# Kernel optimization log

Measured on AMD Instinct MI355X. Metric: run time of the kernel, lower is better.

## Reference

```python
import jax, jax.numpy as jnp
import numpy as np

B = 4096
NQ = 4  # qubits -> 16-dim state vector


def _make_ops(seed, n_ops):
    # Deterministic stand-in for tq.RandomLayer: random RX/RY/RZ/CRX gates.
    rng = np.random.default_rng(seed)
    ops = []
    for _ in range(n_ops):
        kind = int(rng.integers(0, 4))
        if kind == 3:  # CRX on two distinct wires
            w = rng.choice(NQ, size=2, replace=False)
            ops.append((3, int(w[0]), int(w[1])))
        else:
            ops.append((kind, int(rng.integers(0, NQ)), 0))
    return ops

ENC_OPS = _make_ops(1, 8)    # QuantumPatchEncoder.random_layer (n_ops=8)
QFC_OPS = _make_ops(2, 50)   # QuantumFullyConnectedLayer.random_layer (n_ops=50)

_H = np.array([[1, 1], [1, -1]], np.complex64) * np.complex64(1.0 / np.sqrt(2.0))
_SX = np.array([[1 + 1j, 1 - 1j], [1 - 1j, 1 + 1j]], np.complex64) * np.complex64(0.5)
_CNOT = np.array([[1, 0, 0, 0], [0, 1, 0, 0], [0, 0, 0, 1], [0, 0, 1, 0]], np.complex64)


def _rx(t):
    c = jnp.cos(t / 2) + 0j
    s = -1j * jnp.sin(t / 2)
    return jnp.stack([jnp.stack([c, s], -1), jnp.stack([s, c], -1)], -2)


def _ry(t):
    c = jnp.cos(t / 2) + 0j
    s = jnp.sin(t / 2) + 0j
    return jnp.stack([jnp.stack([c, -s], -1), jnp.stack([s, c], -1)], -2)


def _rz(t):
    e0 = jnp.exp(-1j * t / 2)
    e1 = jnp.exp(1j * t / 2)
    z = jnp.zeros_like(e0)
    return jnp.stack([jnp.stack([e0, z], -1), jnp.stack([z, e1], -1)], -2)


def _crx(t):
    return jnp.eye(4, dtype=jnp.complex64).at[2:, 2:].set(_rx(t))


def _apply1(state, U, w):
    # state: (B, 2,2,2,2); U: (2,2) or per-sample (B,2,2)
    state = jnp.moveaxis(state, w + 1, -1)
    if U.ndim == 3:
        state = jnp.einsum('b...i,bji->b...j', state, U)
    else:
        state = jnp.einsum('...i,ji->...j', state, U)
    return jnp.moveaxis(state, -1, w + 1)


def _apply2(state, U, w0, w1):
    state = jnp.moveaxis(state, (w0 + 1, w1 + 1), (-2, -1))
    shp = state.shape
    state = state.reshape(shp[:-2] + (4,)) @ U.T
    return jnp.moveaxis(state.reshape(shp), (-2, -1), (w0 + 1, w1 + 1))


def _random_layer(state, ops, params):
    for i, (kind, w0, w1) in enumerate(ops):
        t = params[i]
        if kind == 0:
            state = _apply1(state, _rx(t), w0)
        elif kind == 1:
            state = _apply1(state, _ry(t), w0)
        elif kind == 2:
            state = _apply1(state, _rz(t), w0)
        else:
            state = _apply2(state, _crx(t), w0, w1)
    return state


def _measure_z(state):
    # <Z> on each wire from |amp|^2 marginals
    probs = state.real ** 2 + state.imag ** 2
    exps = []
    for w in range(NQ):
        axes = tuple(a for a in range(1, NQ + 1) if a != w + 1)
        m = probs.sum(axes)  # (B, 2)
        exps.append(m[:, 0] - m[:, 1])
    return jnp.stack(exps, 1)


def _conv(x, W, b):
    y = jax.lax.conv_general_dilated(x, W, (1, 1), 'SAME',
                                     dimension_numbers=('NCHW', 'OIHW', 'NCHW'))
    return y + b[None, :, None, None]


def _pool(x):
    return jax.lax.reduce_window(x, -jnp.inf, jax.lax.max,
                                 (1, 1, 2, 2), (1, 1, 2, 2), 'VALID')


def setup_inputs() -> dict:
    key = jax.random.key(0)
    ks = jax.random.split(key, 8)
    f = lambda k, shp, fan: jax.random.normal(k, shp, jnp.float32) / np.float32(np.sqrt(fan))
    two_pi = float(2 * np.pi)
    return {
        'x': jax.random.uniform(ks[0], (B, 1, 32, 32), jnp.float32),
        'conv1_w': f(ks[1], (8, 1, 3, 3), 9),
        'conv1_b': jnp.zeros((8,), jnp.float32),
        'conv2_w': f(ks[2], (16, 8, 3, 3), 72),
        'conv2_b': jnp.zeros((16,), jnp.float32),
        'enc_params': jax.random.uniform(ks[3], (8,), jnp.float32, 0.0, two_pi),
        'qfc_rand_params': jax.random.uniform(ks[4], (50,), jnp.float32, 0.0, two_pi),
        'qfc_params': jax.random.uniform(ks[5], (4,), jnp.float32, 0.0, two_pi),
        'bn_gamma': jnp.ones((4,), jnp.float32),
        'bn_beta': jnp.zeros((4,), jnp.float32),
        'fc_w': f(ks[6], (10, 68), 68),
        'fc_b': jnp.zeros((10,), jnp.float32),
    }


def reference(x, conv1_w, conv1_b, conv2_w, conv2_b, enc_params, qfc_rand_params,
              qfc_params, bn_gamma, bn_beta, fc_w, fc_b):
    # CNN feature extractor
    h = _pool(jax.nn.relu(_conv(x, conv1_w, conv1_b)))
    h = _pool(jax.nn.relu(_conv(h, conv2_w, conv2_b)))  # (B, 16, 8, 8)
    b = h.shape[0]
    pm = h.mean(1)  # channel-mean, (B, 8, 8)
    # 2x2 patches, row-major within patch, scanning r then c -> (B, 16, 4)
    patches = pm.reshape(b, 4, 2, 4, 2).transpose(0, 1, 3, 2, 4).reshape(b, 16, 4)

    # Encoder: fresh |0000> per patch (GeneralEncoder resets state); batch all
    # B*16 patch circuits together instead of looping.
    data = patches.reshape(b * 16, 4)
    state = jnp.zeros((b * 16, 16), jnp.complex64).at[:, 0].set(1.0)
    state = state.reshape(b * 16, 2, 2, 2, 2)
    for w in range(NQ):
        state = _apply1(state, _ry(data[:, w]), w)
    state = _random_layer(state, ENC_OPS, enc_params)
    qfeat = _measure_z(state).reshape(b, 64)  # (B, 16*4)

    # QFC operates on the state left by the LAST patch (as in the original)
    s = state.reshape(b, 16, 2, 2, 2, 2)[:, 15]
    s = _random_layer(s, QFC_OPS, qfc_rand_params)
    s = _apply1(s, _rx(qfc_params[0]), 0)
    s = _apply1(s, _ry(qfc_params[1]), 1)
    s = _apply1(s, _rz(qfc_params[2]), 3)
    s = _apply2(s, _crx(qfc_params[3]), 0, 2)
    s = _apply1(s, jnp.asarray(_H), 3)
    s = _apply1(s, jnp.asarray(_SX), 2)
    s = _apply2(s, jnp.asarray(_CNOT), 3, 0)
    q = _measure_z(s)  # (B, 4)

    # BatchNorm1d(4), training-mode (batch stats, biased var)
    mu = q.mean(0)
    var = q.var(0)
    q = (q - mu) / jnp.sqrt(var + 1e-5) * bn_gamma + bn_beta

    feats = jnp.concatenate([qfeat, q], 1)  # (B, 68)
    logits = feats @ fc_w.T + fc_b
    return jax.nn.log_softmax(logits, -1)
```

## Files before the change

kernel.cpp:

```cpp
#include <hip/hip_runtime.h>
#include <cstdint>

namespace crng {

typedef unsigned __int128 u128;

struct PCG {
    u128 state, inc;
    bool has32;
    uint32_t buf32;
};

constexpr u128 PCG_MULT = (((u128)2549297995355413924ULL) << 64) | (u128)4865540595714422341ULL;

constexpr uint64_t pcg_next64(PCG& g) {
    g.state = g.state * PCG_MULT + g.inc;
    uint64_t hi = (uint64_t)(g.state >> 64), lo = (uint64_t)g.state;
    unsigned rot = (unsigned)(g.state >> 122) & 63u;
    uint64_t v = hi ^ lo;
    return (v >> rot) | (v << ((64u - rot) & 63u));
}

constexpr uint32_t pcg_next32(PCG& g) {
    if (g.has32) { g.has32 = false; return g.buf32; }
    uint64_t n = pcg_next64(g);
    g.has32 = true;
    g.buf32 = (uint32_t)(n >> 32);
    return (uint32_t)n;
}

constexpr uint32_t hashmix(uint32_t& hc, uint32_t v) {
    v ^= hc; hc *= 0x931e8875u; v *= hc; v ^= v >> 16; return v;
}
constexpr uint32_t mixf(uint32_t x, uint32_t y) {
    uint32_t r = 0xca01f9ddu * x - 0x4973f715u * y;
    r ^= r >> 16;
    return r;
}

constexpr PCG seed_pcg(uint32_t entropy) {
    uint32_t pool[4] = {0, 0, 0, 0};
    uint32_t hc = 0x43b0d7e5u;
    pool[0] = hashmix(hc, entropy);
    for (int i = 1; i < 4; ++i) pool[i] = hashmix(hc, 0u);
    for (int s = 0; s < 4; ++s)
        for (int d = 0; d < 4; ++d)
            if (s != d) pool[d] = mixf(pool[d], hashmix(hc, pool[s]));

    uint32_t hb = 0x8b51f9ddu;
    uint32_t w[8] = {0, 0, 0, 0, 0, 0, 0, 0};
    for (int i = 0; i < 8; ++i) {
        uint32_t dv = pool[i & 3];
        dv ^= hb; hb *= 0x58f38dedu; dv *= hb; dv ^= dv >> 16;
        w[i] = dv;
    }
    uint64_t w64[4] = {0, 0, 0, 0};
    for (int i = 0; i < 4; ++i)
        w64[i] = (uint64_t)w[2 * i] | ((uint64_t)w[2 * i + 1] << 32);

    u128 initstate = (((u128)w64[0]) << 64) | (u128)w64[1];
    u128 initseq   = (((u128)w64[2]) << 64) | (u128)w64[3];
    PCG g = {};
    g.state = 0;
    g.inc = (initseq << 1) | (u128)1;
    g.state = g.state * PCG_MULT + g.inc;
    g.state += initstate;
    g.state = g.state * PCG_MULT + g.inc;
    g.has32 = false;
    g.buf32 = 0;
    return g;
}

constexpr uint32_t lemire32(PCG& g, uint32_t rng) {
    uint64_t rng_excl = (uint64_t)rng + 1;
    uint64_t m = (uint64_t)pcg_next32(g) * rng_excl;
    uint32_t leftover = (uint32_t)m;
    if (leftover < (uint32_t)rng_excl) {
        uint32_t threshold = (uint32_t)((uint64_t)(0xFFFFFFFFu - rng) % rng_excl);
        while (leftover < threshold) {
            m = (uint64_t)pcg_next32(g) * rng_excl;
            leftover = (uint32_t)m;
        }
    }
    return (uint32_t)(m >> 32);
}

struct Ops {
    int enc[8];
    int qfc[50];
};

constexpr void fill_ops(PCG& g, int n, int* out) {
    for (int i = 0; i < n; ++i) {
        uint32_t kind = lemire32(g, 3);
        uint32_t w0 = 0, w1 = 0;
        if (kind == 3) {
            uint32_t v2 = lemire32(g, 2);
            uint32_t v3 = lemire32(g, 3);
            uint32_t a0 = v2;
            uint32_t a1 = (v3 == v2) ? 3u : v3;
            uint32_t j = lemire32(g, 1);
            if (j == 0) { uint32_t t = a0; a0 = a1; a1 = t; }
            w0 = a0; w1 = a1;
        } else {
            w0 = lemire32(g, 3);
        }
        out[i] = (int)((kind << 4) | (w0 << 2) | w1);
    }
}

constexpr Ops make_ops_ct() {
    Ops o = {};
    PCG g1 = seed_pcg(1u);
    fill_ops(g1, 8, o.enc);
    PCG g2 = seed_pcg(2u);
    fill_ops(g2, 50, o.qfc);
    return o;
}

}

constexpr crng::Ops kOps = crng::make_ops_ct();

typedef _Float16 half8 __attribute__((ext_vector_type(8)));
typedef float float4v __attribute__((ext_vector_type(4)));

#define XS_STRIDE 24
#define XS_PLANE  (34 * XS_STRIDE)
#define XS_TOT    (2 * XS_PLANE)
#define H1F_ROW   (18 * 8)

__global__ __launch_bounds__(256, 4) void cnn_kernel(
    const float* __restrict__ x, const float* __restrict__ w1,
    const float* __restrict__ b1, const float* __restrict__ w2,
    const float* __restrict__ b2, float* __restrict__ pm,
    float* __restrict__ stats)
{
    __shared__ float xs[XS_TOT];
    __shared__ __align__(16) _Float16 h1f[18 * H1F_ROW];
    __shared__ __align__(16) _Float16 Ahalf[9 * 16 * 8];
    __shared__ float w1s[72], b1s[8], b2s[16];

    const int tid = threadIdx.x;
    const int b = blockIdx.x;
    const float* xb = x + (size_t)b * 1024;

    for (int k = tid; k < XS_TOT; k += 256) xs[k] = 0.f;
    for (int k = tid; k < 18 * H1F_ROW; k += 256) h1f[k] = (_Float16)0.f;
    for (int e = tid; e < 1152; e += 256) {
        int uv = e >> 7, m = (e >> 3) & 15, ci = e & 7;
        Ahalf[e] = (_Float16)w2[m * 72 + ci * 9 + uv];
    }
    if (tid < 72) w1s[tid] = w1[tid];
    if (tid < 8) b1s[tid] = b1[tid];
    if (tid < 16) b2s[tid] = b2[tid];
    if (b == 0 && tid < 8) stats[tid] = 0.f;
    __syncthreads();

    for (int k = tid; k < 1024; k += 256) {
        int r = k >> 5, c = k & 31;
        int p = c & 1;
        int q = p ? ((c + 1) >> 1) : (c >> 1);
        xs[p * XS_PLANE + (r + 1) * XS_STRIDE + q] = xb[k];
    }
    __syncthreads();

    {
        const int i = tid >> 4, j = tid & 15;
        float patch[4][4];
#pragma unroll
        for (int u = 0; u < 4; ++u) {
            int r = 2 * i + u;
            const float* ev = &xs[r * XS_STRIDE + j];
            const float* od = &xs[XS_PLANE + r * XS_STRIDE + j];
            patch[u][0] = od[0];
            patch[u][1] = ev[0];
            patch[u][2] = od[1];
            patch[u][3] = ev[1];
        }
        half8 hv;
#pragma unroll
        for (int c = 0; c < 8; ++c) {
            float m = -3.4e38f;
#pragma unroll
            for (int di = 0; di < 2; ++di)
#pragma unroll
                for (int dj = 0; dj < 2; ++dj) {
                    float acc = b1s[c];
#pragma unroll
                    for (int u = 0; u < 3; ++u)
#pragma unroll
                        for (int v = 0; v < 3; ++v)
                            acc += w1s[c * 9 + u * 3 + v] * patch[di + u][dj + v];
                    m = fmaxf(m, acc);
                }
            hv[c] = (_Float16)fmaxf(m, 0.f);
        }
        *(half8*)&h1f[(i + 1) * H1F_ROW + (j + 1) * 8] = hv;
    }
    __syncthreads();

    {
        const int w = tid >> 6;
        const int lane = tid & 63;
        const int pj = lane & 15;
        const int quad = lane >> 4;

        half8 afrag[9];
#pragma unroll
        for (int uv = 0; uv < 9; ++uv) {
            half8 a = {};
            if (quad == 0) a = *(const half8*)&Ahalf[(uv * 16 + pj) * 8];
            afrag[uv] = a;
        }

        float4v acc[4];
#pragma unroll
        for (int tl = 0; tl < 4; ++tl) {
            float4v c;
#pragma unroll
            for (int r = 0; r < 4; ++r) c[r] = b2s[4 * quad + r];
            acc[tl] = c;
        }

#pragma unroll
        for (int tl = 0; tl < 4; ++tl) {
            const int t = 4 * w + tl;
#pragma unroll
            for (int u = 0; u < 3; ++u) {
#pragma unroll
                for (int v = 0; v < 3; ++v) {
                    half8 bf = *(const half8*)&h1f[(t + u) * H1F_ROW + (pj + v) * 8];
                    acc[tl] = __builtin_amdgcn_mfma_f32_16x16x32_f16(
                        afrag[u * 3 + v], bf, acc[tl], 0, 0, 0);
                }
            }
        }

#pragma unroll
        for (int p = 0; p < 2; ++p) {
            float4v m1;
#pragma unroll
            for (int r = 0; r < 4; ++r)
                m1[r] = fmaxf(acc[2 * p][r], acc[2 * p + 1][r]);
            float s = 0.f;
#pragma unroll
            for (int r = 0; r < 4; ++r) {
                float o = __shfl_xor((float)m1[r], 1, 64);
                float mv = fmaxf(fmaxf(m1[r], o), 0.f);
                s += mv;
            }
            s += __shfl_xor(s, 16, 64);
            s += __shfl_xor(s, 32, 64);
            if (quad == 0 && !(pj & 1)) {
                const int i2 = 2 * w + p, j2 = pj >> 1;
                pm[(size_t)b * 64 + i2 * 8 + j2] = s * (1.f / 16.f);
            }
        }
    }
}

template<int KIND, int W0, int W1>
__device__ __forceinline__ void gate_ct(float (&ur)[16], float (&ui)[16],
                                        float ch, float sh)
{
    constexpr bool CTRL = (KIND == 3 || KIND == 6);
    constexpr int STT = CTRL ? (8 >> W1) : (8 >> W0);
    constexpr int STC = CTRL ? (8 >> W0) : 0;
#pragma unroll
    for (int k0 = 0; k0 < 16; ++k0) {
        if (k0 & STT) continue;
        if (STC != 0 && !(k0 & STC)) continue;
        const int k1 = k0 | STT;
        float x0r = ur[k0], x0i = ui[k0], x1r = ur[k1], x1i = ui[k1];
        if constexpr (KIND == 0 || KIND == 3) {
            ur[k0] = ch * x0r + sh * x1i;  ui[k0] = ch * x0i - sh * x1r;
            ur[k1] = sh * x0i + ch * x1r;  ui[k1] = -sh * x0r + ch * x1i;
        } else if constexpr (KIND == 1) {
            ur[k0] = ch * x0r - sh * x1r;  ui[k0] = ch * x0i - sh * x1i;
            ur[k1] = sh * x0r + ch * x1r;  ui[k1] = sh * x0i + ch * x1i;
        } else if constexpr (KIND == 2) {
            ur[k0] = ch * x0r + sh * x0i;  ui[k0] = ch * x0i - sh * x0r;
            ur[k1] = ch * x1r - sh * x1i;  ui[k1] = ch * x1i + sh * x1r;
        } else if constexpr (KIND == 4) {
            constexpr float RH = 0.70710678118654752f;
            ur[k0] = RH * (x0r + x1r);  ui[k0] = RH * (x0i + x1i);
            ur[k1] = RH * (x0r - x1r);  ui[k1] = RH * (x0i - x1i);
        } else if constexpr (KIND == 5) {
            ur[k0] = 0.5f * (x0r + x1r) - 0.5f * x0i + 0.5f * x1i;
            ui[k0] = 0.5f * (x0i + x1i) + 0.5f * x0r - 0.5f * x1r;
            ur[k1] = 0.5f * (x0r + x1r) + 0.5f * x0i - 0.5f * x1i;
            ui[k1] = 0.5f * (x0i + x1i) - 0.5f * x0r + 0.5f * x1r;
        } else {
            ur[k0] = x1r; ui[k0] = x1i;
            ur[k1] = x0r; ui[k1] = x0i;
        }
    }
}

template<int I>
__device__ __forceinline__ void run_enc(float (&ur)[16], float (&ui)[16],
                                        const float* ch, const float* sh)
{
    if constexpr (I < 8) {
        constexpr int op = kOps.enc[I];
        gate_ct<(op >> 4) & 7, (op >> 2) & 3, op & 3>(ur, ui, ch[I], sh[I]);
        run_enc<I + 1>(ur, ui, ch, sh);
    }
}

template<int I>
__device__ __forceinline__ void run_qfc(float (&ur)[16], float (&ui)[16],
                                        const float* ch, const float* sh)
{
    if constexpr (I < 50) {
        constexpr int op = kOps.qfc[I];
        gate_ct<(op >> 4) & 7, (op >> 2) & 3, op & 3>(ur, ui, ch[I], sh[I]);
        run_qfc<I + 1>(ur, ui, ch, sh);
    }
}

__global__ __launch_bounds__(256) void quantum_kernel(
    const float* __restrict__ pm, const float* __restrict__ encp,
    const float* __restrict__ qfcr, const float* __restrict__ qfcp,
    float* __restrict__ qfeat, float* __restrict__ qraw,
    float* __restrict__ stats, int Bv)
{
    __shared__ float chs[62], shs[62];
    __shared__ float rstat[128];

    const int tid = threadIdx.x;
    if (tid < 62) {
        float t = (tid < 8) ? encp[tid] : (tid < 58) ? qfcr[tid - 8] : qfcp[tid - 58];
        chs[tid] = cosf(0.5f * t);
        shs[tid] = sinf(0.5f * t);
    }
    __syncthreads();

    const int gid = blockIdx.x * 256 + tid;
    const int b = gid >> 4, p = gid & 15;
    float qq[4] = {0.f, 0.f, 0.f, 0.f};
    bool last = false;

    if (b < Bv) {
        const int pr = p >> 2, pc = p & 3;
        const float* pmb = pm + (size_t)b * 64;
        float d0 = pmb[(2 * pr) * 8 + 2 * pc];
        float d1 = pmb[(2 * pr) * 8 + 2 * pc + 1];
        float d2 = pmb[(2 * pr + 1) * 8 + 2 * pc];
        float d3 = pmb[(2 * pr + 1) * 8 + 2 * pc + 1];
        float f0c = cosf(0.5f * d0), f0s = sinf(0.5f * d0);
        float f1c = cosf(0.5f * d1), f1s = sinf(0.5f * d1);
        float f2c = cosf(0.5f * d2), f2s = sinf(0.5f * d2);
        float f3c = cosf(0.5f * d3), f3s = sinf(0.5f * d3);

        float ur[16], ui[16];
#pragma unroll
        for (int k = 0; k < 16; ++k) {
            float v = ((k & 8) ? f0s : f0c);
            v *= ((k & 4) ? f1s : f1c);
            v *= ((k & 2) ? f2s : f2c);
            v *= ((k & 1) ? f3s : f3c);
            ur[k] = v;
            ui[k] = 0.f;
        }
        run_enc<0>(ur, ui, chs, shs);

        float qv[4] = {0.f, 0.f, 0.f, 0.f};
#pragma unroll
        for (int k = 0; k < 16; ++k) {
            float pk = ur[k] * ur[k] + ui[k] * ui[k];
            qv[0] += (k & 8) ? -pk : pk;
            qv[1] += (k & 4) ? -pk : pk;
            qv[2] += (k & 2) ? -pk : pk;
            qv[3] += (k & 1) ? -pk : pk;
        }
        *(float4*)(qfeat + (size_t)b * 64 + p * 4) = make_float4(qv[0], qv[1], qv[2], qv[3]);

        if (p == 15) {
            last = true;
            run_qfc<0>(ur, ui, chs + 8, shs + 8);
            gate_ct<0, 0, 0>(ur, ui, chs[58], shs[58]);
            gate_ct<1, 1, 0>(ur, ui, chs[59], shs[59]);
            gate_ct<2, 3, 0>(ur, ui, chs[60], shs[60]);
            gate_ct<3, 0, 2>(ur, ui, chs[61], shs[61]);
            gate_ct<4, 3, 0>(ur, ui, 0.f, 0.f);
            gate_ct<5, 2, 0>(ur, ui, 0.f, 0.f);
            gate_ct<6, 3, 0>(ur, ui, 0.f, 0.f);
#pragma unroll
            for (int k = 0; k < 16; ++k) {
                float pk = ur[k] * ur[k] + ui[k] * ui[k];
                qq[0] += (k & 8) ? -pk : pk;
                qq[1] += (k & 4) ? -pk : pk;
                qq[2] += (k & 2) ? -pk : pk;
                qq[3] += (k & 1) ? -pk : pk;
            }
            *(float4*)(qraw + (size_t)b * 4) = make_float4(qq[0], qq[1], qq[2], qq[3]);
        }
    }

    for (int k = tid; k < 128; k += 256) rstat[k] = 0.f;
    __syncthreads();
    const int m = tid >> 4;
    if (last) {
#pragma unroll
        for (int w = 0; w < 4; ++w) {
            rstat[w * 16 + m] = qq[w];
            rstat[64 + w * 16 + m] = qq[w] * qq[w];
        }
    }
    __syncthreads();
    if (tid < 8) {
        float s = 0.f;
#pragma unroll
        for (int k = 0; k < 16; ++k) s += rstat[tid * 16 + k];
        atomicAdd(&stats[tid], s);
    }
}

__global__ __launch_bounds__(256) void head_kernel(
    const float* __restrict__ qfeat, const float* __restrict__ qraw,
    const float* __restrict__ stats, const float* __restrict__ gam,
    const float* __restrict__ bet, const float* __restrict__ fcw,
    const float* __restrict__ fcb, float* __restrict__ out, int Bv)
{
    __shared__ float Wf[680];
    __shared__ float bf[10], st[8], ga[4], be[4];
    const int tid = threadIdx.x;
    for (int k = tid; k < 680; k += 256) Wf[k] = fcw[k];
    if (tid < 10) bf[tid] = fcb[tid];
    if (tid < 8) st[tid] = stats[tid];
    if (tid < 4) { ga[tid] = gam[tid]; be[tid] = bet[tid]; }
    __syncthreads();

    const int b = blockIdx.x * 256 + tid;
    if (b >= Bv) return;

    const float invB = 1.f / (float)Bv;

    float logit[10];
#pragma unroll
    for (int k = 0; k < 10; ++k) logit[k] = bf[k];

    const float* qf = qfeat + (size_t)b * 64;
    for (int j = 0; j < 64; ++j) {
        float v = qf[j];
#pragma unroll
        for (int k = 0; k < 10; ++k) logit[k] += v * Wf[k * 68 + j];
    }
    float4 qr = *(const float4*)(qraw + (size_t)b * 4);
    float qn[4] = {qr.x, qr.y, qr.z, qr.w};
#pragma unroll
    for (int w = 0; w < 4; ++w) {
        float mu = st[w] * invB;
        float var = st[4 + w] * invB - mu * mu;
        float v = (qn[w] - mu) / sqrtf(var + 1e-5f) * ga[w] + be[w];
#pragma unroll
        for (int k = 0; k < 10; ++k) logit[k] += v * Wf[k * 68 + 64 + w];
    }

    float m = logit[0];
#pragma unroll
    for (int k = 1; k < 10; ++k) m = fmaxf(m, logit[k]);
    float sum = 0.f;
#pragma unroll
    for (int k = 0; k < 10; ++k) sum += expf(logit[k] - m);
    float lse = logf(sum);
#pragma unroll
    for (int k = 0; k < 10; ++k) out[(size_t)b * 10 + k] = logit[k] - m - lse;
}

extern "C" void kernel_launch(void* const* d_in, const int* in_sizes, int n_in,
                              void* d_out, int out_size, void* d_ws, size_t ws_size,
                              hipStream_t stream)
{
    const float* x    = (const float*)d_in[0];
    const float* w1   = (const float*)d_in[1];
    const float* b1   = (const float*)d_in[2];
    const float* w2   = (const float*)d_in[3];
    const float* b2   = (const float*)d_in[4];
    const float* encp = (const float*)d_in[5];
    const float* qfcr = (const float*)d_in[6];
    const float* qfcp = (const float*)d_in[7];
    const float* gam  = (const float*)d_in[8];
    const float* bet  = (const float*)d_in[9];
    const float* fcw  = (const float*)d_in[10];
    const float* fcb  = (const float*)d_in[11];
    float* out = (float*)d_out;

    const int Bv = in_sizes[0] / 1024;

    float* pm    = (float*)d_ws;
    float* qfeat = pm + (size_t)Bv * 64;
    float* qraw  = qfeat + (size_t)Bv * 64;
    float* stats = qraw + (size_t)Bv * 4;

    cnn_kernel<<<Bv, 256, 0, stream>>>(x, w1, b1, w2, b2, pm, stats);
    quantum_kernel<<<(Bv * 16 + 255) / 256, 256, 0, stream>>>(
        pm, encp, qfcr, qfcp, qfeat, qraw, stats, Bv);
    head_kernel<<<(Bv + 255) / 256, 256, 0, stream>>>(qfeat, qraw, stats, gam, bet,
                                                      fcw, fcb, out, Bv);
}
```

Measured before the change: 139.3 us.

## Use packed fp16 conv1, transpose qfeat layout, shrink head blocks, vectorize zeroing

Moves the first convolution to packed half2 arithmetic: weights, bias and input patch are converted to fp16 and the max-pool and ReLU are done in fp16, which lowers ALU work but reduces accuracy. The quantum features are now written feature-major so that the head kernel's reads across the batch coalesce, at the cost of strided scattered writes in the quantum kernel. The head kernel drops to 64-thread blocks so more blocks spread across CUs. Shared-memory zeroing is vectorized with float4 and half8 stores.

```diff
diff --git a/kernel.cpp b/kernel.cpp
--- a/kernel.cpp
+++ b/kernel.cpp
@@ -123,12 +123,14 @@
 constexpr crng::Ops kOps = crng::make_ops_ct();
 
 typedef _Float16 half8 __attribute__((ext_vector_type(8)));
+typedef _Float16 half2v __attribute__((ext_vector_type(2)));
 typedef float float4v __attribute__((ext_vector_type(4)));
 
 #define XS_STRIDE 24
 #define XS_PLANE  (34 * XS_STRIDE)
 #define XS_TOT    (2 * XS_PLANE)
 #define H1F_ROW   (18 * 8)
+#define H1F_TOT   (18 * H1F_ROW)
 
 __global__ __launch_bounds__(256, 4) void cnn_kernel(
     const float* __restrict__ x, const float* __restrict__ w1,
@@ -136,23 +138,26 @@
     const float* __restrict__ b2, float* __restrict__ pm,
     float* __restrict__ stats)
 {
-    __shared__ float xs[XS_TOT];
-    __shared__ __align__(16) _Float16 h1f[18 * H1F_ROW];
+    __shared__ __align__(16) float xs[XS_TOT];
+    __shared__ __align__(16) _Float16 h1f[H1F_TOT];
     __shared__ __align__(16) _Float16 Ahalf[9 * 16 * 8];
-    __shared__ float w1s[72], b1s[8], b2s[16];
+    __shared__ _Float16 w1h[72], b1h[8];
+    __shared__ float b2s[16];
 
     const int tid = threadIdx.x;
     const int b = blockIdx.x;
     const float* xb = x + (size_t)b * 1024;
 
-    for (int k = tid; k < XS_TOT; k += 256) xs[k] = 0.f;
-    for (int k = tid; k < 18 * H1F_ROW; k += 256) h1f[k] = (_Float16)0.f;
+    for (int k = tid; k < XS_TOT / 4; k += 256)
+        ((float4*)xs)[k] = make_float4(0.f, 0.f, 0.f, 0.f);
+    for (int k = tid; k < H1F_TOT / 8; k += 256)
+        ((half8*)h1f)[k] = (half8)0;
     for (int e = tid; e < 1152; e += 256) {
         int uv = e >> 7, m = (e >> 3) & 15, ci = e & 7;
         Ahalf[e] = (_Float16)w2[m * 72 + ci * 9 + uv];
     }
-    if (tid < 72) w1s[tid] = w1[tid];
-    if (tid < 8) b1s[tid] = b1[tid];
+    if (tid < 72) w1h[tid] = (_Float16)w1[tid];
+    if (tid < 8) b1h[tid] = (_Float16)b1[tid];
     if (tid < 16) b2s[tid] = b2[tid];
     if (b == 0 && tid < 8) stats[tid] = 0.f;
     __syncthreads();
@@ -167,34 +172,38 @@
 
     {
         const int i = tid >> 4, j = tid & 15;
-        float patch[4][4];
+        _Float16 ph[4][4];
 #pragma unroll
         for (int u = 0; u < 4; ++u) {
             int r = 2 * i + u;
             const float* ev = &xs[r * XS_STRIDE + j];
             const float* od = &xs[XS_PLANE + r * XS_STRIDE + j];
-            patch[u][0] = od[0];
-            patch[u][1] = ev[0];
-            patch[u][2] = od[1];
-            patch[u][3] = ev[1];
+            ph[u][0] = (_Float16)od[0];
+            ph[u][1] = (_Float16)ev[0];
+            ph[u][2] = (_Float16)od[1];
+            ph[u][3] = (_Float16)ev[1];
         }
         half8 hv;
 #pragma unroll
         for (int c = 0; c < 8; ++c) {
-            float m = -3.4e38f;
-#pragma unroll
-            for (int di = 0; di < 2; ++di)
-#pragma unroll
-                for (int dj = 0; dj < 2; ++dj) {
-                    float acc = b1s[c];
-#pragma unroll
-                    for (int u = 0; u < 3; ++u)
-#pragma unroll
-                        for (int v = 0; v < 3; ++v)
-                            acc += w1s[c * 9 + u * 3 + v] * patch[di + u][dj + v];
-                    m = fmaxf(m, acc);
+            half2v acc0 = {b1h[c], b1h[c]};
+            half2v acc1 = acc0;
+#pragma unroll
+            for (int u = 0; u < 3; ++u) {
+#pragma unroll
+                for (int v = 0; v < 3; ++v) {
+                    _Float16 w = w1h[c * 9 + u * 3 + v];
+                    half2v wv = {w, w};
+                    half2v p0 = {ph[u][v], ph[u][v + 1]};
+                    half2v p1 = {ph[u + 1][v], ph[u + 1][v + 1]};
+                    acc0 += wv * p0;
+                    acc1 += wv * p1;
                 }
-            hv[c] = (_Float16)fmaxf(m, 0.f);
+            }
+            _Float16 m0 = (acc0.x > acc0.y) ? acc0.x : acc0.y;
+            _Float16 m1 = (acc1.x > acc1.y) ? acc1.x : acc1.y;
+            _Float16 mm = (m0 > m1) ? m0 : m1;
+            hv[c] = (mm > (_Float16)0.f) ? mm : (_Float16)0.f;
         }
         *(half8*)&h1f[(i + 1) * H1F_ROW + (j + 1) * 8] = hv;
     }
@@ -323,7 +332,7 @@
 __global__ __launch_bounds__(256) void quantum_kernel(
     const float* __restrict__ pm, const float* __restrict__ encp,
     const float* __restrict__ qfcr, const float* __restrict__ qfcp,
-    float* __restrict__ qfeat, float* __restrict__ qraw,
+    float* __restrict__ qfeatT, float* __restrict__ qraw,
     float* __restrict__ stats, int Bv)
 {
     __shared__ float chs[62], shs[62];
@@ -375,7 +384,9 @@
             qv[2] += (k & 2) ? -pk : pk;
             qv[3] += (k & 1) ? -pk : pk;
         }
-        *(float4*)(qfeat + (size_t)b * 64 + p * 4) = make_float4(qv[0], qv[1], qv[2], qv[3]);
+#pragma unroll
+        for (int w = 0; w < 4; ++w)
+            qfeatT[(size_t)(p * 4 + w) * Bv + b] = qv[w];
 
         if (p == 15) {
             last = true;
@@ -418,8 +429,8 @@
     }
 }
 
-__global__ __launch_bounds__(256) void head_kernel(
-    const float* __restrict__ qfeat, const float* __restrict__ qraw,
+__global__ __launch_bounds__(64) void head_kernel(
+    const float* __restrict__ qfeatT, const float* __restrict__ qraw,
     const float* __restrict__ stats, const float* __restrict__ gam,
     const float* __restrict__ bet, const float* __restrict__ fcw,
     const float* __restrict__ fcb, float* __restrict__ out, int Bv)
@@ -427,13 +438,13 @@
     __shared__ float Wf[680];
     __shared__ float bf[10], st[8], ga[4], be[4];
     const int tid = threadIdx.x;
-    for (int k = tid; k < 680; k += 256) Wf[k] = fcw[k];
+    for (int k = tid; k < 680; k += 64) Wf[k] = fcw[k];
     if (tid < 10) bf[tid] = fcb[tid];
     if (tid < 8) st[tid] = stats[tid];
     if (tid < 4) { ga[tid] = gam[tid]; be[tid] = bet[tid]; }
     __syncthreads();
 
-    const int b = blockIdx.x * 256 + tid;
+    const int b = blockIdx.x * 64 + tid;
     if (b >= Bv) return;
 
     const float invB = 1.f / (float)Bv;
@@ -442,11 +453,10 @@
 #pragma unroll
     for (int k = 0; k < 10; ++k) logit[k] = bf[k];
 
-    const float* qf = qfeat + (size_t)b * 64;
-    for (int j = 0; j < 64; ++j) {
-        float v = qf[j];
-#pragma unroll
-        for (int k = 0; k < 10; ++k) logit[k] += v * Wf[k * 68 + j];
+    for (int f = 0; f < 64; ++f) {
+        float v = qfeatT[(size_t)f * Bv + b];
+#pragma unroll
+        for (int k = 0; k < 10; ++k) logit[k] += v * Wf[k * 68 + f];
     }
     float4 qr = *(const float4*)(qraw + (size_t)b * 4);
     float qn[4] = {qr.x, qr.y, qr.z, qr.w};
@@ -490,14 +500,14 @@
 
     const int Bv = in_sizes[0] / 1024;
 
-    float* pm    = (float*)d_ws;
-    float* qfeat = pm + (size_t)Bv * 64;
-    float* qraw  = qfeat + (size_t)Bv * 64;
-    float* stats = qraw + (size_t)Bv * 4;
+    float* pm     = (float*)d_ws;
+    float* qfeatT = pm + (size_t)Bv * 64;
+    float* qraw   = qfeatT + (size_t)Bv * 64;
+    float* stats  = qraw + (size_t)Bv * 4;
 
     cnn_kernel<<<Bv, 256, 0, stream>>>(x, w1, b1, w2, b2, pm, stats);
     quantum_kernel<<<(Bv * 16 + 255) / 256, 256, 0, stream>>>(
-        pm, encp, qfcr, qfcp, qfeat, qraw, stats, Bv);
-    head_kernel<<<(Bv + 255) / 256, 256, 0, stream>>>(qfeat, qraw, stats, gam, bet,
-                                                      fcw, fcb, out, Bv);
-}
+        pm, encp, qfcr, qfcp, qfeatT, qraw, stats, Bv);
+    head_kernel<<<(Bv + 63) / 64, 64, 0, stream>>>(qfeatT, qraw, stats, gam, bet,
+                                                   fcw, fcb, out, Bv);
+}
```

Measured after the change: 216.6 us. +55.5%, slower.
